# Optimization experiments

Measured on AMD Instinct MI355X. Metric: run time of the kernel, lower is better.

The kernel has to match this reference:

```python
import jax, jax.numpy as jnp
import numpy as np

N, D_IN, HID, OUT, E = 131072, 256, 1024, 1, 100


def setup_inputs() -> dict:
    key = jax.random.key(0)
    k = jax.random.split(key, 7)
    return {
        "x": jax.random.normal(k[0], (N, D_IN), dtype=jnp.float32),
        "W1": jax.random.normal(k[1], (HID, D_IN), dtype=jnp.float32) * 0.05,
        "b1": jax.random.normal(k[2], (HID,), dtype=jnp.float32) * 0.05,
        "We": jax.random.normal(k[3], (E, OUT, HID), dtype=jnp.float32) * 0.05,
        "be": jax.random.normal(k[4], (E, OUT), dtype=jnp.float32) * 0.05,
        "num": jax.random.randint(k[5], (N,), 0, E, dtype=jnp.int64),
        "c": jax.random.randint(k[6], (E,), 0, E, dtype=jnp.int64),
    }


def reference(x, W1, b1, We, be, num, c):
    # feature: Linear + ReLU  -> [N, HID]
    h = jax.nn.relu(x @ W1.T + b1)
    # per-sample expert index: c[num[i]]
    e = c[num]                                  # [N]
    Wg = We[e]                                  # [N, OUT, HID] gathered expert weights
    bg = be[e]                                  # [N, OUT]
    y = jnp.einsum('noh,nh->no', Wg, h) + bg    # per-sample expert linear
    return jax.nn.sigmoid(y)
```

## Files before the change

### kernel.cpp

```cpp
#include <hip/hip_runtime.h>
#include <stdint.h>

#define N_SAMP 131072
#define DIN    256
#define HIDN   1024
#define BROWS  128
#define NTHREADS 256
#define NCHUNK 16

typedef __attribute__((ext_vector_type(8))) short short8;
typedef __attribute__((ext_vector_type(4))) float f32x4;

__device__ __forceinline__ unsigned short f2bf(float f) {
  unsigned u = __float_as_uint(f);
  u += 0x7fffu + ((u >> 16) & 1u);
  return (unsigned short)(u >> 16);
}

__device__ __forceinline__ short8 pack8(float4 a, float4 b) {
  short8 r;
  r[0] = (short)f2bf(a.x); r[1] = (short)f2bf(a.y);
  r[2] = (short)f2bf(a.z); r[3] = (short)f2bf(a.w);
  r[4] = (short)f2bf(b.x); r[5] = (short)f2bf(b.y);
  r[6] = (short)f2bf(b.z); r[7] = (short)f2bf(b.w);
  return r;
}

__global__ __launch_bounds__(256) void w1_pack(const float* __restrict__ W1,
                                               unsigned short* __restrict__ o) {
  int idx = blockIdx.x * 256 + threadIdx.x;
  int l  = idx & 63;
  int nt = (idx >> 6) & 3;
  int s  = (idx >> 8) & 7;
  int ch = idx >> 11;
  int col = ch * 64 + nt * 16 + (l & 15);
  int k0  = s * 32 + (l >> 4) * 8;
  const float* src = W1 + (size_t)col * DIN + k0;
  float4 f0 = *(const float4*)src;
  float4 f1 = *(const float4*)(src + 4);
  ((short8*)o)[idx] = pack8(f0, f1);
}

template <bool WBF>
__global__ __launch_bounds__(NTHREADS, 2) void fused_kernel(
    const float* __restrict__ x,
    const float* __restrict__ W1f,
    const unsigned short* __restrict__ W1p,
    const float* __restrict__ b1,
    const float* __restrict__ We,
    const float* __restrict__ be,
    const int* __restrict__ num,
    const int* __restrict__ c,
    float* __restrict__ out)
{
  __shared__ unsigned short Wt[2][16384];
  __shared__ int e_sh[BROWS];

  const int tid  = threadIdx.x;
  const int lane = tid & 63;
  const int w    = tid >> 6;
  const int n    = lane & 15;
  const int quad = lane >> 4;
  const int R0   = blockIdx.x * BROWS;

  if (tid < BROWS) e_sh[tid] = c[num[R0 + tid]];

  short8 afr[2][8];
  {
    const float* xr0 = x + (size_t)(R0 + w * 32 + n) * DIN + quad * 8;
#pragma unroll
    for (int t = 0; t < 2; ++t) {
      const float* xr = xr0 + (size_t)t * 16 * DIN;
#pragma unroll
      for (int s = 0; s < 8; ++s) {
        float4 f0 = *(const float4*)(xr + s * 32);
        float4 f1 = *(const float4*)(xr + s * 32 + 4);
        afr[t][s] = pack8(f0, f1);
      }
    }
  }

  if (WBF) {
#pragma unroll
    for (int j = 0; j < 8; ++j) {
      int inst = w * 8 + j;
      const unsigned short* g = W1p + inst * 512 + lane * 8;
      __builtin_amdgcn_global_load_lds(
          (const __attribute__((address_space(1))) unsigned int*)g,
          (__attribute__((address_space(3))) unsigned int*)(&Wt[0][0] + inst * 512),
          16, 0, 0);
    }
  } else {
#pragma unroll
    for (int j = 0; j < 8; ++j) {
      int id = tid + j * NTHREADS;
      int l = id & 63, f = id >> 6;
      int nt = f & 3, s = f >> 2;
      int col = nt * 16 + (l & 15);
      int k0  = s * 32 + (l >> 4) * 8;
      const float* gs = W1f + (size_t)col * DIN + k0;
      float4 f0 = *(const float4*)gs;
      float4 f1 = *(const float4*)(gs + 4);
      *(short8*)&Wt[0][f * 512 + l * 8] = pack8(f0, f1);
    }
  }

  __syncthreads();

  int eoff[2][4];
#pragma unroll
  for (int t = 0; t < 2; ++t)
#pragma unroll
    for (int r = 0; r < 4; ++r)
      eoff[t][r] = e_sh[w * 32 + t * 16 + quad * 4 + r] * HIDN;

  float yacc[2][4] = {{0.f, 0.f, 0.f, 0.f}, {0.f, 0.f, 0.f, 0.f}};

  int buf = 0;
  for (int ch = 0; ch < NCHUNK; ++ch) {
    if (ch + 1 < NCHUNK) {
      if (WBF) {
        const unsigned short* Wg = W1p + (size_t)(ch + 1) * 16384;
        unsigned short* db = &Wt[buf ^ 1][0];
#pragma unroll
        for (int j = 0; j < 8; ++j) {
          int inst = w * 8 + j;
          const unsigned short* g = Wg + inst * 512 + lane * 8;
          __builtin_amdgcn_global_load_lds(
              (const __attribute__((address_space(1))) unsigned int*)g,
              (__attribute__((address_space(3))) unsigned int*)(db + inst * 512),
              16, 0, 0);
        }
      } else {
        const float* Wc = W1f + (size_t)(ch + 1) * 64 * DIN;
#pragma unroll
        for (int j = 0; j < 8; ++j) {
          int id = tid + j * NTHREADS;
          int l = id & 63, f = id >> 6;
          int nt = f & 3, s = f >> 2;
          int col = nt * 16 + (l & 15);
          int k0  = s * 32 + (l >> 4) * 8;
          const float* gs = Wc + (size_t)col * DIN + k0;
          float4 f0 = *(const float4*)gs;
          float4 f1 = *(const float4*)(gs + 4);
          *(short8*)&Wt[buf ^ 1][f * 512 + l * 8] = pack8(f0, f1);
        }
      }
    }

    const char* Bbase = (const char*)&Wt[buf][0] + lane * 16;
    f32x4 acc[2][4];
#pragma unroll
    for (int t = 0; t < 2; ++t)
#pragma unroll
      for (int nt = 0; nt < 4; ++nt)
        acc[t][nt] = (f32x4){0.f, 0.f, 0.f, 0.f};

#pragma unroll
    for (int s = 0; s < 8; ++s) {
      short8 bfr[4];
#pragma unroll
      for (int nt = 0; nt < 4; ++nt)
        bfr[nt] = *(const short8*)(Bbase + (s * 4 + nt) * 1024);
#pragma unroll
      for (int t = 0; t < 2; ++t)
#pragma unroll
        for (int nt = 0; nt < 4; ++nt)
          acc[t][nt] = __builtin_amdgcn_mfma_f32_16x16x32_bf16(
              afr[t][s], bfr[nt], acc[t][nt], 0, 0, 0);
    }

#pragma unroll
    for (int nt = 0; nt < 4; ++nt) {
      int col = ch * 64 + nt * 16 + n;
      float bv = b1[col];
      const float* Wec = We + col;
#pragma unroll
      for (int t = 0; t < 2; ++t)
#pragma unroll
        for (int r = 0; r < 4; ++r) {
          float h = acc[t][nt][r] + bv;
          h = fmaxf(h, 0.f);
          yacc[t][r] = fmaf(h, Wec[eoff[t][r]], yacc[t][r]);
        }
    }

    __syncthreads();
    buf ^= 1;
  }

#pragma unroll
  for (int t = 0; t < 2; ++t)
#pragma unroll
    for (int r = 0; r < 4; ++r) {
      float v = yacc[t][r];
      v += __shfl_xor(v, 1);
      v += __shfl_xor(v, 2);
      v += __shfl_xor(v, 4);
      v += __shfl_xor(v, 8);
      yacc[t][r] = v;
    }

  if (n == 0) {
#pragma unroll
    for (int t = 0; t < 2; ++t)
#pragma unroll
      for (int r = 0; r < 4; ++r) {
        int row = R0 + w * 32 + t * 16 + quad * 4 + r;
        float yy = yacc[t][r] + be[eoff[t][r] >> 10];
        out[row] = 1.f / (1.f + __expf(-yy));
      }
  }
}

extern "C" void kernel_launch(void* const* d_in, const int* in_sizes, int n_in,
                              void* d_out, int out_size, void* d_ws, size_t ws_size,
                              hipStream_t stream) {
  const float* x   = (const float*)d_in[0];
  const float* W1  = (const float*)d_in[1];
  const float* b1  = (const float*)d_in[2];
  const float* We  = (const float*)d_in[3];
  const float* be  = (const float*)d_in[4];
  const int*   num = (const int*)d_in[5];
  const int*   c   = (const int*)d_in[6];
  float* out = (float*)d_out;

  const size_t w1p_bytes = (size_t)HIDN * DIN * sizeof(unsigned short);
  const bool usebf = ws_size >= w1p_bytes;
  unsigned short* w1p = (unsigned short*)d_ws;

  if (usebf) {
    w1_pack<<<dim3((HIDN * DIN / 8) / 256), dim3(256), 0, stream>>>(W1, w1p);
    fused_kernel<true><<<dim3(N_SAMP / BROWS), dim3(NTHREADS), 0, stream>>>(
        x, W1, w1p, b1, We, be, num, c, out);
  } else {
    fused_kernel<false><<<dim3(N_SAMP / BROWS), dim3(NTHREADS), 0, stream>>>(
        x, W1, w1p, b1, We, be, num, c, out);
  }
}
```

Baseline: 261.4 us.

## Double rows per block to reuse each W1 chunk across more samples

```diff
diff --git a/kernel.cpp b/kernel.cpp
--- a/kernel.cpp
+++ b/kernel.cpp
@@ -4,7 +4,7 @@
 #define N_SAMP 131072
 #define DIN    256
 #define HIDN   1024
-#define BROWS  128
+#define BROWS  256
 #define NTHREADS 256
 #define NCHUNK 16
 
@@ -42,7 +42,7 @@
 }
 
 template <bool WBF>
-__global__ __launch_bounds__(NTHREADS, 2) void fused_kernel(
+__global__ void fused_kernel(
     const float* __restrict__ x,
     const float* __restrict__ W1f,
     const unsigned short* __restrict__ W1p,
@@ -65,11 +65,11 @@
 
   if (tid < BROWS) e_sh[tid] = c[num[R0 + tid]];
 
-  short8 afr[2][8];
+  short8 afr[4][8];
   {
-    const float* xr0 = x + (size_t)(R0 + w * 32 + n) * DIN + quad * 8;
-#pragma unroll
-    for (int t = 0; t < 2; ++t) {
+    const float* xr0 = x + (size_t)(R0 + w * 64 + n) * DIN + quad * 8;
+#pragma unroll
+    for (int t = 0; t < 4; ++t) {
       const float* xr = xr0 + (size_t)t * 16 * DIN;
 #pragma unroll
       for (int s = 0; s < 8; ++s) {
@@ -107,14 +107,18 @@
 
   __syncthreads();
 
-  int eoff[2][4];
-#pragma unroll
-  for (int t = 0; t < 2; ++t)
+  int eoff[4][4];
+#pragma unroll
+  for (int t = 0; t < 4; ++t)
 #pragma unroll
     for (int r = 0; r < 4; ++r)
-      eoff[t][r] = e_sh[w * 32 + t * 16 + quad * 4 + r] * HIDN;
-
-  float yacc[2][4] = {{0.f, 0.f, 0.f, 0.f}, {0.f, 0.f, 0.f, 0.f}};
+      eoff[t][r] = e_sh[w * 64 + t * 16 + quad * 4 + r] * HIDN;
+
+  float yacc[4][4];
+#pragma unroll
+  for (int t = 0; t < 4; ++t)
+#pragma unroll
+    for (int r = 0; r < 4; ++r) yacc[t][r] = 0.f;
 
   int buf = 0;
   for (int ch = 0; ch < NCHUNK; ++ch) {
@@ -149,40 +153,44 @@
     }
 
     const char* Bbase = (const char*)&Wt[buf][0] + lane * 16;
-    f32x4 acc[2][4];
-#pragma unroll
-    for (int t = 0; t < 2; ++t)
-#pragma unroll
-      for (int nt = 0; nt < 4; ++nt)
-        acc[t][nt] = (f32x4){0.f, 0.f, 0.f, 0.f};
-
-#pragma unroll
-    for (int s = 0; s < 8; ++s) {
-      short8 bfr[4];
-#pragma unroll
-      for (int nt = 0; nt < 4; ++nt)
-        bfr[nt] = *(const short8*)(Bbase + (s * 4 + nt) * 1024);
-#pragma unroll
-      for (int t = 0; t < 2; ++t)
-#pragma unroll
-        for (int nt = 0; nt < 4; ++nt)
-          acc[t][nt] = __builtin_amdgcn_mfma_f32_16x16x32_bf16(
-              afr[t][s], bfr[nt], acc[t][nt], 0, 0, 0);
-    }
-
-#pragma unroll
-    for (int nt = 0; nt < 4; ++nt) {
-      int col = ch * 64 + nt * 16 + n;
-      float bv = b1[col];
-      const float* Wec = We + col;
-#pragma unroll
-      for (int t = 0; t < 2; ++t)
-#pragma unroll
-        for (int r = 0; r < 4; ++r) {
-          float h = acc[t][nt][r] + bv;
-          h = fmaxf(h, 0.f);
-          yacc[t][r] = fmaf(h, Wec[eoff[t][r]], yacc[t][r]);
-        }
+
+#pragma unroll
+    for (int half = 0; half < 2; ++half) {
+      f32x4 acc[4][2];
+#pragma unroll
+      for (int t = 0; t < 4; ++t)
+#pragma unroll
+        for (int nn = 0; nn < 2; ++nn)
+          acc[t][nn] = (f32x4){0.f, 0.f, 0.f, 0.f};
+
+#pragma unroll
+      for (int s = 0; s < 8; ++s) {
+        short8 bfr[2];
+#pragma unroll
+        for (int nn = 0; nn < 2; ++nn)
+          bfr[nn] = *(const short8*)(Bbase + (s * 4 + half * 2 + nn) * 1024);
+#pragma unroll
+        for (int t = 0; t < 4; ++t)
+#pragma unroll
+          for (int nn = 0; nn < 2; ++nn)
+            acc[t][nn] = __builtin_amdgcn_mfma_f32_16x16x32_bf16(
+                afr[t][s], bfr[nn], acc[t][nn], 0, 0, 0);
+      }
+
+#pragma unroll
+      for (int nn = 0; nn < 2; ++nn) {
+        int col = ch * 64 + (half * 2 + nn) * 16 + n;
+        float bv = b1[col];
+        const float* Wec = We + col;
+#pragma unroll
+        for (int t = 0; t < 4; ++t)
+#pragma unroll
+          for (int r = 0; r < 4; ++r) {
+            float h = acc[t][nn][r] + bv;
+            h = fmaxf(h, 0.f);
+            yacc[t][r] = fmaf(h, Wec[eoff[t][r]], yacc[t][r]);
+          }
+      }
     }
 
     __syncthreads();
@@ -190,7 +198,7 @@
   }
 
 #pragma unroll
-  for (int t = 0; t < 2; ++t)
+  for (int t = 0; t < 4; ++t)
 #pragma unroll
     for (int r = 0; r < 4; ++r) {
       float v = yacc[t][r];
@@ -203,10 +211,10 @@
 
   if (n == 0) {
 #pragma unroll
-    for (int t = 0; t < 2; ++t)
+    for (int t = 0; t < 4; ++t)
 #pragma unroll
       for (int r = 0; r < 4; ++r) {
-        int row = R0 + w * 32 + t * 16 + quad * 4 + r;
+        int row = R0 + w * 64 + t * 16 + quad * 4 + r;
         float yy = yacc[t][r] + be[eoff[t][r] >> 10];
         out[row] = 1.f / (1.f + __expf(-yy));
       }
```

Result: slower. 615.5 us (+135.5%).
